# Kernel optimization log

Hardware: AMD Instinct MI355X
Metric: run time of the kernel (lower is better)

The kernel has to match this reference:

```python
import jax, jax.numpy as jnp
import numpy as np
from jax import lax

B, Q, H, W = 2, 2304, 64, 64
ENC_OUT = 64          # encoder out_dim
DIM = 192             # base_dim
HEAD = 8
R = 3
RA = (2 * R + 1) ** 2  # 49 local-window positions
CF = 64                # pe enc_dims // 2 (complex channels)
ENC_DIMS = 2 * CF      # 128
IN_DIM = (DIM + ENC_DIMS) * RA + 2  # 15682
HID = 256


def conv3(x, w, b):
    y = lax.conv_general_dilated(x, w, (1, 1), 'SAME',
                                 dimension_numbers=('NCHW', 'OIHW', 'NCHW'))
    return y + b[None, :, None, None]


def _flat_gather(img, idx):
    # img [B,C,HW], idx [B,...] -> [B,C,...]
    return jax.vmap(lambda f, i: f[:, i])(img, idx)


def gather_nearest(img, c):
    # grid_sample nearest, align_corners=False, zeros padding. c [B,Q,K,2] (y,x)
    Bc, C, Hc, Wc = img.shape
    py = ((c[..., 0] + 1) * Hc - 1) / 2
    px = ((c[..., 1] + 1) * Wc - 1) / 2
    iy = jnp.round(py); ix = jnp.round(px)
    valid = (iy >= 0) & (iy < Hc) & (ix >= 0) & (ix < Wc)
    idx = (jnp.clip(iy, 0, Hc - 1) * Wc + jnp.clip(ix, 0, Wc - 1)).astype(jnp.int32)
    g = _flat_gather(img.reshape(Bc, C, Hc * Wc), idx)  # [B,C,Q,K]
    g = jnp.where(valid[:, None], g, 0.0)
    return g.transpose(0, 2, 3, 1)  # [B,Q,K,C]


def gather_bilinear_zeros(img, c):
    # grid_sample bilinear, align_corners=False, zeros padding. c [B,Q,K,2]
    Bc, C, Hc, Wc = img.shape
    py = ((c[..., 0] + 1) * Hc - 1) / 2
    px = ((c[..., 1] + 1) * Wc - 1) / 2
    y0f = jnp.floor(py); x0f = jnp.floor(px)
    wy = py - y0f; wx = px - x0f
    y0 = y0f.astype(jnp.int32); x0 = x0f.astype(jnp.int32)
    flat = img.reshape(Bc, C, Hc * Wc)
    def corner(yi, xi, w):
        valid = (yi >= 0) & (yi < Hc) & (xi >= 0) & (xi < Wc)
        idx = jnp.clip(yi, 0, Hc - 1) * Wc + jnp.clip(xi, 0, Wc - 1)
        return _flat_gather(flat, idx) * (w * valid)[:, None]
    out = (corner(y0, x0, (1 - wy) * (1 - wx)) + corner(y0, x0 + 1, (1 - wy) * wx)
           + corner(y0 + 1, x0, wy * (1 - wx)) + corner(y0 + 1, x0 + 1, wy * wx))
    return out.transpose(0, 2, 3, 1)


def gather_bilinear_border(img, c):
    # grid_sample bilinear, align_corners=False, border padding. c [B,Q,2]
    Bc, C, Hc, Wc = img.shape
    py = jnp.clip(((c[..., 0] + 1) * Hc - 1) / 2, 0, Hc - 1)
    px = jnp.clip(((c[..., 1] + 1) * Wc - 1) / 2, 0, Wc - 1)
    y0f = jnp.floor(py); x0f = jnp.floor(px)
    wy = py - y0f; wx = px - x0f
    y0 = y0f.astype(jnp.int32); x0 = x0f.astype(jnp.int32)
    y1 = jnp.minimum(y0 + 1, Hc - 1); x1 = jnp.minimum(x0 + 1, Wc - 1)
    flat = img.reshape(Bc, C, Hc * Wc)
    g = lambda yi, xi: _flat_gather(flat, yi * Wc + xi)  # [B,C,Q]
    out = (g(y0, x0) * ((1 - wy) * (1 - wx))[:, None]
           + g(y0, x1) * ((1 - wy) * wx)[:, None]
           + g(y1, x0) * (wy * (1 - wx))[:, None]
           + g(y1, x1) * (wy * wx)[:, None])
    return out.transpose(0, 2, 1)  # [B,Q,C]


def _forward(inp, coord, cell, enc_w, enc_b, qw, qb, kw, kb, vw, vb, fw, fb,
             pbw, pbb, pew, w1, b1, w2, b2):
    feat = conv3(inp, enc_w, enc_b)            # encoder (simplified)
    fq = conv3(feat, qw, qb); fk = conv3(feat, kw, kb)
    fv = conv3(feat, vw, vb); ff = conv3(feat, fw, fb)
    Bq, Qn = coord.shape[:2]
    Hf, Wf = feat.shape[-2:]
    dk = DIM // HEAD
    c = jnp.clip(coord, -1 + 1e-6, 1 - 1e-6)[:, :, None, :]   # [B,Q,1,2]
    # nearest feature-grid pixel-center coordinates (= grid_sample nearest of coord_lr)
    iy = jnp.round(((c[..., 0] + 1) * Hf - 1) / 2)
    ix = jnp.round(((c[..., 1] + 1) * Wf - 1) / 2)
    ck0 = jnp.stack([-1 + (2 * iy + 1) / Hf, -1 + (2 * ix + 1) / Wf], axis=-1)
    dh = jnp.linspace(-R, R, 2 * R + 1) * 2 / Hf
    dw = jnp.linspace(-R, R, 2 * R + 1) * 2 / Wf
    delta = jnp.stack(jnp.meshgrid(dh, dw, indexing='ij'), axis=-1).reshape(1, 1, RA, 2)
    ck = ck0 + delta                                          # [B,Q,49,2]
    q_ = gather_bilinear_zeros(fq, c)[:, :, 0].reshape(Bq, Qn, HEAD, dk)
    k_ = gather_nearest(fk, ck).reshape(Bq, Qn, RA, HEAD, dk)
    v_ = gather_nearest(fv, ck).reshape(Bq, Qn, RA, HEAD, dk)
    fr = gather_nearest(ff, ck)                               # [B,Q,49,CF]
    hw = jnp.array([Hf, Wf], dtype=coord.dtype)
    rel = (coord[:, :, None, :] - ck) * hw                    # [B,Q,49,2]
    rel_cell = cell * hw
    sim = jnp.einsum('bqhd,bqkhd->bqkh', q_, k_) / np.sqrt(dk).astype(np.float32)
    pb = rel @ pbw + pbb                                      # positional bias [B,Q,49,HEAD]
    attn = jax.nn.softmax(sim + pb, axis=2)                   # softmax over the 49 window slots
    attn_map = attn[0, 10, :, 0].reshape(2 * R + 1, 2 * R + 1, 1)
    v_weighted = (v_ * attn[..., None]).reshape(Bq, Qn, RA, DIM)
    frc = jnp.fft.fft2(fr.reshape(Bq, Qn, 2 * R + 1, 2 * R + 1, CF),
                       axes=(2, 3), norm='ortho').reshape(Bq, Qn, RA, CF)
    phase = rel @ pew                                         # Fourier PE: exp(i*phase)
    enc = lax.complex(jnp.cos(phase), jnp.sin(phase)) * frc
    enc = jnp.stack([enc.real, enc.imag], axis=-1).reshape(Bq, Qn, RA, ENC_DIMS)
    out = jnp.concatenate([v_weighted, enc], axis=-1).reshape(Bq, Qn, -1)
    out = jnp.concatenate([out, rel_cell], axis=-1)           # [B,Q,IN_DIM]
    pred = jax.nn.relu(out @ w1 + b1) @ w2 + b2               # imnet MLP
    ret = pred + gather_bilinear_border(inp, coord)           # global residual
    return ret, attn_map


def setup_inputs() -> dict:
    key = jax.random.key(0)
    ks = jax.random.split(key, 20)
    def n(k, shape, s=0.05):
        return jax.random.normal(k, shape, dtype=jnp.float32) * s
    inp = jax.random.normal(ks[0], (B, 3, H, W), dtype=jnp.float32)
    coord = jax.random.uniform(ks[1], (B, Q, 2), minval=-1.0, maxval=1.0, dtype=jnp.float32)
    cell = jnp.full((B, Q, 2), 2.0 / 128, dtype=jnp.float32)
    return {
        'inp': inp, 'coord': coord, 'cell': cell,
        'enc_w': n(ks[2], (ENC_OUT, 3, 3, 3)), 'enc_b': n(ks[3], (ENC_OUT,)),
        'qw': n(ks[4], (DIM, ENC_OUT, 3, 3)), 'qb': n(ks[5], (DIM,)),
        'kw': n(ks[6], (DIM, ENC_OUT, 3, 3)), 'kb': n(ks[7], (DIM,)),
        'vw': n(ks[8], (DIM, ENC_OUT, 3, 3)), 'vb': n(ks[9], (DIM,)),
        'fw': n(ks[10], (CF, ENC_OUT, 3, 3)), 'fb': n(ks[11], (CF,)),
        'pbw': n(ks[12], (2, HEAD), 0.5), 'pbb': n(ks[13], (HEAD,), 0.5),
        'pew': n(ks[14], (2, CF), 0.5),
        'w1': n(ks[15], (IN_DIM, HID), 0.01), 'b1': n(ks[16], (HID,)),
        'w2': n(ks[17], (HID, 3), 0.05), 'b2': n(ks[18], (3,)),
    }


def reference(inp, coord, cell, enc_w, enc_b, qw, qb, kw, kb, vw, vb, fw, fb,
              pbw, pbb, pew, w1, b1, w2, b2):
    return _forward(inp, coord, cell, enc_w, enc_b, qw, qb, kw, kb, vw, vb,
                    fw, fb, pbw, pbb, pew, w1, b1, w2, b2)
```

## Files before the change

### kernel.cpp

```cpp
#include <hip/hip_runtime.h>

typedef unsigned short u16t;
typedef unsigned int   u32t;
typedef __attribute__((ext_vector_type(8))) short short8;
typedef __attribute__((ext_vector_type(4))) float f32x4;

#define B_    2
#define QN    2304
#define NQ    4608
#define HWS   64
#define ENCC  64
#define DIMC  192
#define NHEAD 8
#define DKH   24
#define RAW   49
#define CFC   64
#define FRP   68
#define CMAP  640
#define KCONV 576
#define INDIM 15682
#define KPAD  16128
#define HIDN  256
#define PIX   8192
#define SPLITK 12
#define KSLICE (KPAD/SPLITK)

__device__ __forceinline__ float b2f(u16t u){ u32t v=((u32t)u)<<16; return __builtin_bit_cast(float,v); }
__device__ __forceinline__ u16t f2b(float f){ u32t v=__builtin_bit_cast(u32t,f); return (u16t)((v + 0x7FFFu + ((v>>16)&1u))>>16); }

#define GLOAD16(SRC, DST) __builtin_amdgcn_global_load_lds( \
  (const __attribute__((address_space(1))) unsigned int*)(const void*)(SRC), \
  (__attribute__((address_space(3))) unsigned int*)(void*)(DST), 16, 0, 0)

__global__ __launch_bounds__(256) void k_enc(const float* __restrict__ inp, const float* __restrict__ ew,
                      const float* __restrict__ eb, u16t* __restrict__ feat){
  int i = blockIdx.x*256+threadIdx.x;
  if(i>=B_*HWS*HWS*ENCC) return;
  int oc=i&63, x=(i>>6)&63, y=(i>>12)&63, b=i>>18;
  float acc = eb[oc];
  for(int c=0;c<3;c++)
    for(int dy=0;dy<3;dy++){
      int yy=y+dy-1; if(yy<0||yy>=HWS) continue;
      for(int dx=0;dx<3;dx++){
        int xx=x+dx-1; if(xx<0||xx>=HWS) continue;
        acc += inp[((b*3+c)*HWS+yy)*HWS+xx] * ew[((oc*3+c)*3+dy)*3+dx];
      }
    }
  feat[i]=f2b(acc);
}

__global__ __launch_bounds__(256) void k_w1t(const float* __restrict__ w1, u16t* __restrict__ w1t){
  __shared__ u16t t[64][65];
  int kb = blockIdx.x*64, nb = blockIdx.y*64;
  for(int i=threadIdx.x;i<4096;i+=256){
    int k=i>>6, n=i&63; int gk=kb+k;
    t[k][n] = (gk<INDIM) ? f2b(w1[(size_t)gk*HIDN + nb + n]) : (u16t)0;
  }
  __syncthreads();
  for(int i=threadIdx.x;i<4096;i+=256){
    int n=i>>6, k=i&63;
    w1t[(size_t)(nb+n)*KPAD + kb + k] = t[k][n];
  }
}

__global__ __launch_bounds__(256) void k_wconv(const float* qw,const float* kw,const float* vw,const float* fw,
                        const float* qb,const float* kb_,const float* vb,const float* fb,
                        u16t* __restrict__ wct, float* __restrict__ bias){
  int i = blockIdx.x*256+threadIdx.x;
  if(i < CMAP*KCONV){
    int oc=i/KCONV, kk=i%KCONV;
    int ic=kk&63, tap=kk>>6;
    const float* w; int ol=oc;
    if(oc<192) w=qw;
    else if(oc<384){w=kw; ol=oc-192;}
    else if(oc<576){w=vw; ol=oc-384;}
    else {w=fw; ol=oc-576;}
    wct[(size_t)oc*KCONV + kk] = f2b(w[(ol*64+ic)*9 + tap]);
  }
  if(i<CMAP){
    bias[i] = (i<192)? qb[i] : (i<384? kb_[i-192] : (i<576? vb[i-384] : fb[i-576]));
  }
}

__global__ __launch_bounds__(256) void k_im2col(const u16t* __restrict__ feat, u16t* __restrict__ A){
  int i = blockIdx.x*256+threadIdx.x;
  if(i>=PIX*72) return;
  int k8=i%72, pix=i/72;
  int tap=k8/8, ic8=(k8&7)<<3;
  int x=pix&63, y=(pix>>6)&63, b=pix>>12;
  int yy=y+tap/3-1, xx=x+tap%3-1;
  uint4 v;
  if(yy>=0&&yy<HWS&&xx>=0&&xx<HWS) v = *(const uint4*)&feat[(size_t)(((b*HWS+yy)*HWS+xx)*ENCC)+ic8];
  else v = make_uint4(0u,0u,0u,0u);
  *(uint4*)&A[(size_t)pix*KCONV + tap*64 + ic8] = v;
}

__global__ __launch_bounds__(256) void k_gemm128(const u16t* __restrict__ A, int lda,
    const u16t* __restrict__ BT, int ldb, const float* __restrict__ bias,
    void* __restrict__ Cout, int ldc, int kslice, int mode){
  __shared__ __align__(16) u16t As[128*64];
  __shared__ __align__(16) u16t Bs[128*64];
  int m0 = blockIdx.x*128, n0 = blockIdx.y*128;
  int tid = threadIdx.x;
  int wave = tid>>6, lane = tid&63;
  int wm = wave>>1, wn = wave&1;
  int kg = lane>>4, l16 = lane&15;
  int kbeg = blockIdx.z*kslice, kend = kbeg+kslice;
  f32x4 acc[4][4] = {};
  for(int k0=kbeg;k0<kend;k0+=64){
    __syncthreads();
    #pragma unroll
    for(int j=0;j<4;j++){
      int seg = (wave*4+j)*64 + lane;
      int row = seg>>3, qp = seg&7;
      int q = qp ^ (row&7);
      GLOAD16(&A [(size_t)(m0+row)*lda + k0 + q*8], &As[(wave*4+j)*512]);
      GLOAD16(&BT[(size_t)(n0+row)*ldb + k0 + q*8], &Bs[(wave*4+j)*512]);
    }
    __syncthreads();
    #pragma unroll
    for(int kk=0;kk<2;kk++){
      int ks = kk*4 + kg;
      short8 a[4], b[4];
      #pragma unroll
      for(int mf=0;mf<4;mf++){
        int row = wm*64+mf*16+l16;
        a[mf] = *(const short8*)&As[row*64 + (ks^(row&7))*8];
      }
      #pragma unroll
      for(int nf=0;nf<4;nf++){
        int row = wn*64+nf*16+l16;
        b[nf] = *(const short8*)&Bs[row*64 + (ks^(row&7))*8];
      }
      #pragma unroll
      for(int mf=0;mf<4;mf++)
        #pragma unroll
        for(int nf=0;nf<4;nf++)
          acc[mf][nf] = __builtin_amdgcn_mfma_f32_16x16x32_bf16(a[mf], b[nf], acc[mf][nf], 0,0,0);
    }
  }
  int l4 = lane>>4;
  if(mode==0){
    u16t* C16 = (u16t*)Cout;
    #pragma unroll
    for(int mf=0;mf<4;mf++){
      #pragma unroll
      for(int nf=0;nf<4;nf++){
        #pragma unroll
        for(int r=0;r<4;r++){
          int gm = m0 + wm*64 + mf*16 + l4*4 + r;
          int gn = n0 + wn*64 + nf*16 + l16;
          C16[(size_t)gm*ldc+gn] = f2b(acc[mf][nf][r] + bias[gn]);
        }
      }
    }
  } else {
    u16t* C16 = (u16t*)Cout + (size_t)blockIdx.z * (size_t)(gridDim.x*128) * ldc;
    #pragma unroll
    for(int mf=0;mf<4;mf++){
      #pragma unroll
      for(int nf=0;nf<4;nf++){
        #pragma unroll
        for(int r=0;r<4;r++){
          int gm = m0 + wm*64 + mf*16 + l4*4 + r;
          int gn = n0 + wn*64 + nf*16 + l16;
          C16[(size_t)gm*ldc+gn] = f2b(acc[mf][nf][r]);
        }
      }
    }
  }
}

__global__ __launch_bounds__(256) void k_redout(const u16t* __restrict__ hidp, const float* __restrict__ b1,
                      const float* __restrict__ w2, const float* __restrict__ b2v,
                      const float* __restrict__ inp, const float* __restrict__ coord,
                      float* __restrict__ outp, int M, int q0){
  int i = blockIdx.x*256+threadIdx.x;
  if(i>=M*64) return;
  int q=i>>6, lane=i&63, n4=lane*4;
  f32x4 acc = *(const f32x4*)&b1[n4];
  for(int s=0;s<SPLITK;s++){
    uint2 t = *(const uint2*)&hidp[((size_t)s*M + q)*HIDN + n4];
    acc.x += b2f((u16t)t.x); acc.y += b2f((u16t)(t.x>>16));
    acc.z += b2f((u16t)t.y); acc.w += b2f((u16t)(t.y>>16));
  }
  float h0=fmaxf(acc.x,0.f), h1=fmaxf(acc.y,0.f), h2=fmaxf(acc.z,0.f), h3=fmaxf(acc.w,0.f);
  float p0 = h0*w2[n4*3+0] + h1*w2[(n4+1)*3+0] + h2*w2[(n4+2)*3+0] + h3*w2[(n4+3)*3+0];
  float p1 = h0*w2[n4*3+1] + h1*w2[(n4+1)*3+1] + h2*w2[(n4+2)*3+1] + h3*w2[(n4+3)*3+1];
  float p2 = h0*w2[n4*3+2] + h1*w2[(n4+1)*3+2] + h2*w2[(n4+2)*3+2] + h3*w2[(n4+3)*3+2];
  #pragma unroll
  for(int m=1;m<64;m<<=1){
    p0 += __shfl_xor(p0, m);
    p1 += __shfl_xor(p1, m);
    p2 += __shfl_xor(p2, m);
  }
  if(lane<3){
    int qg = q0 + q;
    int j = lane;
    float accj = (j==0? p0 : (j==1? p1 : p2)) + b2v[j];
    int b=qg/QN;
    float cy=coord[qg*2], cx=coord[qg*2+1];
    float py=fminf(fmaxf(((cy+1.f)*64.f-1.f)*0.5f,0.f),63.f);
    float px=fminf(fmaxf(((cx+1.f)*64.f-1.f)*0.5f,0.f),63.f);
    float y0f=floorf(py), x0f=floorf(px);
    float wy=py-y0f, wx=px-x0f;
    int y0=(int)y0f, x0=(int)x0f;
    int y1=min(y0+1,63), x1=min(x0+1,63);
    const float* ip=&inp[(size_t)(b*3+j)*4096];
    float g00=ip[y0*64+x0], g01=ip[y0*64+x1];
    float g10=ip[y1*64+x0], g11=ip[y1*64+x1];
    float res=g00*(1.f-wy)*(1.f-wx)+g01*(1.f-wy)*wx+g10*wy*(1.f-wx)+g11*wy*wx;
    outp[qg*3+j]=accj+res;
  }
}

__global__ __launch_bounds__(256,8) void k_feat(const float* __restrict__ coord, const float* __restrict__ cell,
                       const u16t* __restrict__ maps, const float* __restrict__ pbw,
                       const float* __restrict__ pbb, const float* __restrict__ pew,
                       u16t* __restrict__ F, float* __restrict__ outAttn, int q0){
  __shared__ float q_lds[DIMC];
  __shared__ float relsy[RAW], relsx[RAW];
  __shared__ int   wbase[RAW];
  __shared__ float sa[RAW][NHEAD];
  __shared__ float fr_lds[RAW*FRP];
  __shared__ float c7[7], s7[7];
  __shared__ float pewf0[CFC], pewf1[CFC];
  __shared__ float pbwf0[NHEAD], pbwf1[NHEAD], pbbf[NHEAD];

  int qg = q0 + blockIdx.x;
  int b  = qg / QN;
  int tid = threadIdx.x;
  float cy = coord[qg*2], cx = coord[qg*2+1];
  const float lo = -1.0f + 1e-6f, hi = 1.0f - 1e-6f;
  float ccy = fminf(fmaxf(cy,lo),hi), ccx = fminf(fmaxf(cx,lo),hi);
  float pyq = ((ccy+1.f)*64.f - 1.f)*0.5f, pxq = ((ccx+1.f)*64.f - 1.f)*0.5f;
  int iy = (int)rintf(pyq), ix = (int)rintf(pxq);

  if(tid < RAW){
    int ki = tid/7, kj = tid%7;
    int yy = iy + ki - 3, xx = ix + kj - 3;
    wbase[tid] = (yy>=0&&yy<64&&xx>=0&&xx<64) ? ((b*64+yy)*64+xx)*CMAP : -1;
    float ck_y = (-1.f + (float)(2*iy+1)*(1.f/64.f)) + (float)(ki-3)*(2.f/64.f);
    float ck_x = (-1.f + (float)(2*ix+1)*(1.f/64.f)) + (float)(kj-3)*(2.f/64.f);
    relsy[tid] = (cy - ck_y)*64.f;
    relsx[tid] = (cx - ck_x)*64.f;
  }
  if(tid<7){ float ang = -6.283185307179586f * (float)tid / 7.f; c7[tid]=cosf(ang); s7[tid]=sinf(ang); }
  if(tid<CFC){ pewf0[tid]=pew[tid]; pewf1[tid]=pew[CFC+tid]; }
  if(tid<NHEAD){ pbwf0[tid]=pbw[tid]; pbwf1[tid]=pbw[NHEAD+tid]; pbbf[tid]=pbb[tid]; }
  __syncthreads();

  if(tid < DIMC){
    float y0f=floorf(pyq), x0f=floorf(pxq);
    float wy=pyq-y0f, wx=pxq-x0f;
    int y0=(int)y0f, x0=(int)x0f;
    float acc=0.f;
    for(int ty=0;ty<2;ty++) for(int tx=0;tx<2;tx++){
      int yy=y0+ty, xx=x0+tx;
      if(yy<0||yy>=64||xx<0||xx>=64) continue;
      float w=(ty? wy:1.f-wy)*(tx? wx:1.f-wx);
      acc += w * b2f(maps[(size_t)((b*64+yy)*64+xx)*CMAP + tid]);
    }
    q_lds[tid]=acc;
  }
  for(int i=tid;i<RAW*8;i+=256){
    int k=i>>3, c8=(i&7)<<3;
    int base=wbase[k];
    f32x4 lo4={0.f,0.f,0.f,0.f}, hi4={0.f,0.f,0.f,0.f};
    if(base>=0){
      uint4 t = *(const uint4*)&maps[(size_t)base + 576 + c8];
      lo4 = f32x4{b2f((u16t)t.x), b2f((u16t)(t.x>>16)), b2f((u16t)t.y), b2f((u16t)(t.y>>16))};
      hi4 = f32x4{b2f((u16t)t.z), b2f((u16t)(t.z>>16)), b2f((u16t)t.w), b2f((u16t)(t.w>>16))};
    }
    *(f32x4*)&fr_lds[k*FRP+c8]   = lo4;
    *(f32x4*)&fr_lds[k*FRP+c8+4] = hi4;
  }
  __syncthreads();

  for(int i=tid;i<RAW*NHEAD;i+=256){
    int k=i>>3, h=i&7;
    int base=wbase[k];
    float dot=0.f;
    if(base>=0){
      const u16t* p = &maps[(size_t)base + DIMC + h*DKH];
      for(int c8=0;c8<3;c8++){
        uint4 t = *(const uint4*)&p[c8*8];
        u32t a4[4]={t.x,t.y,t.z,t.w};
        for(int j=0;j<4;j++){
          dot += q_lds[h*DKH + c8*8 + 2*j]   * b2f((u16t)a4[j]);
          dot += q_lds[h*DKH + c8*8 + 2*j+1] * b2f((u16t)(a4[j]>>16));
        }
      }
    }
    sa[k][h] = dot/sqrtf(24.f) + relsy[k]*pbwf0[h] + relsx[k]*pbwf1[h] + pbbf[h];
  }
  __syncthreads();

  if(tid < 64){
    int h = tid>>3, sub = tid&7;
    float m = -1e30f;
    for(int k=sub;k<RAW;k+=8) m = fmaxf(m, sa[k][h]);
    #pragma unroll
    for(int mm=1;mm<8;mm<<=1) m = fmaxf(m, __shfl_xor(m, mm));
    float s = 0.f;
    for(int k=sub;k<RAW;k+=8){ float e=__expf(sa[k][h]-m); sa[k][h]=e; s+=e; }
    #pragma unroll
    for(int mm=1;mm<8;mm<<=1) s += __shfl_xor(s, mm);
    float inv = 1.f/s;
    for(int k=sub;k<RAW;k+=8) sa[k][h]*=inv;
  }
  __syncthreads();
  if(qg==10 && tid<RAW) outAttn[tid] = sa[tid][0];

  size_t frow = (size_t)(qg-q0)*KPAD;
  for(int i=tid;i<RAW*24;i+=256){
    int k=i/24, c8=(i%24)*8;
    int base=wbase[k];
    u32t o[4]={0,0,0,0};
    if(base>=0){
      uint4 t = *(const uint4*)&maps[(size_t)base + 384 + c8];
      u32t a4[4]={t.x,t.y,t.z,t.w};
      for(int j=0;j<4;j++){
        int c0=c8+2*j;
        u16t r0=f2b(b2f((u16t)a4[j])      * sa[k][ c0   /DKH]);
        u16t r1=f2b(b2f((u16t)(a4[j]>>16))* sa[k][(c0+1)/DKH]);
        o[j] = (u32t)r0 | ((u32t)r1<<16);
      }
    }
    *(uint4*)&F[frow + (size_t)k*320 + c8] = make_uint4(o[0],o[1],o[2],o[3]);
  }
  for(int idx=INDIM-2+tid; idx<KPAD; idx+=256){
    u16t v=0;
    if(idx==15680) v=f2b(cell[qg*2]*64.f);
    else if(idx==15681) v=f2b(cell[qg*2+1]*64.f);
    F[frow+idx]=v;
  }

  #pragma unroll
  for(int pp=0;pp<2;pp++){
    int p = tid + pp*256;
    if(p < 448){
      int v_ = p>>6, c = p&63;
      float Gr[7], Gi[7];
      #pragma unroll
      for(int a_=0;a_<7;a_++){
        float re=0.f, im=0.f;
        #pragma unroll
        for(int bb=0;bb<7;bb++){
          float f=fr_lds[(a_*7+bb)*FRP+c];
          int m=(v_*bb)%7;
          re += f*c7[m]; im += f*s7[m];
        }
        Gr[a_]=re; Gi[a_]=im;
      }
      float pw0=pewf0[c], pw1=pewf1[c];
      #pragma unroll
      for(int u=0;u<7;u++){
        int k = u*7 + v_;
        float tr=0.f, ti=0.f;
        #pragma unroll
        for(int a_=0;a_<7;a_++){
          int m=(u*a_)%7;
          float cc=c7[m], ss=s7[m];
          tr += Gr[a_]*cc - Gi[a_]*ss;
          ti += Gr[a_]*ss + Gi[a_]*cc;
        }
        tr*=(1.f/7.f); ti*=(1.f/7.f);
        float ph = relsy[k]*pw0 + relsx[k]*pw1;
        float sp, cp; __sincosf(ph, &sp, &cp);
        float er = cp*tr - sp*ti, ei = cp*ti + sp*tr;
        u32t pk = (u32t)f2b(er) | ((u32t)f2b(ei)<<16);
        *(u32t*)&F[frow + (size_t)k*320 + 192 + 2*c] = pk;
      }
    }
  }
}

__global__ __launch_bounds__(256) void k_mark(float* __restrict__ outp, int n, float val){
  int i = blockIdx.x*256+threadIdx.x;
  if(i<n) outp[i]=val;
}

extern "C" void kernel_launch(void* const* d_in, const int* in_sizes, int n_in,
                              void* d_out, int out_size, void* d_ws, size_t ws_size,
                              hipStream_t stream){
  int I_inp, I_coord, I_cell, I_encw, I_encb, I_qw, I_qb, I_kw, I_kb, I_vw, I_vb,
      I_fw, I_fb, I_pbw, I_pbb, I_pew, I_w1, I_b1, I_w2, I_b2;
  bool dictOrder = (n_in==20 && in_sizes[0]==24576 && in_sizes[1]==9216 && in_sizes[3]==1728
                    && in_sizes[5]==110592 && in_sizes[16]==4014592 && in_sizes[19]==3);
  bool sortOrder = (n_in==20 && in_sizes[0]==256 && in_sizes[1]==3 && in_sizes[8]==24576
                    && in_sizes[10]==110592 && in_sizes[18]==4014592 && in_sizes[19]==768);
  if(dictOrder){
    I_inp=0; I_coord=1; I_cell=2; I_encw=3; I_encb=4; I_qw=5; I_qb=6; I_kw=7; I_kb=8;
    I_vw=9; I_vb=10; I_fw=11; I_fb=12; I_pbw=13; I_pbb=14; I_pew=15; I_w1=16; I_b1=17; I_w2=18; I_b2=19;
  } else if(sortOrder){
    I_b1=0; I_b2=1; I_cell=2; I_coord=3; I_encb=4; I_encw=5; I_fb=6; I_fw=7; I_inp=8;
    I_kb=9; I_kw=10; I_pbb=11; I_pbw=12; I_pew=13; I_qb=14; I_qw=15; I_vb=16; I_vw=17; I_w1=18; I_w2=19;
  } else {
    float mark = (float)(n_in==20 ? in_sizes[0] : 1000000+n_in);
    k_mark<<<dim3((out_size+255)/256), dim3(256), 0, stream>>>((float*)d_out, out_size, mark);
    return;
  }

  const float* inp  =(const float*)d_in[I_inp];
  const float* coord=(const float*)d_in[I_coord];
  const float* cell =(const float*)d_in[I_cell];
  const float* enc_w=(const float*)d_in[I_encw];
  const float* enc_b=(const float*)d_in[I_encb];
  const float* qw=(const float*)d_in[I_qw];
  const float* qb=(const float*)d_in[I_qb];
  const float* kw=(const float*)d_in[I_kw];
  const float* kbp=(const float*)d_in[I_kb];
  const float* vw=(const float*)d_in[I_vw];
  const float* vb=(const float*)d_in[I_vb];
  const float* fw=(const float*)d_in[I_fw];
  const float* fb=(const float*)d_in[I_fb];
  const float* pbw=(const float*)d_in[I_pbw];
  const float* pbb=(const float*)d_in[I_pbb];
  const float* pew=(const float*)d_in[I_pew];
  const float* w1=(const float*)d_in[I_w1];
  const float* b1=(const float*)d_in[I_b1];
  const float* w2=(const float*)d_in[I_w2];
  const float* b2v=(const float*)d_in[I_b2];
  float* outp=(float*)d_out;

  char* ws=(char*)d_ws;
  size_t off=0;
  auto alloc=[&](size_t bytes){ size_t o=off; off=(off+bytes+255)&~(size_t)255; return o; };
  size_t o_feat = alloc((size_t)PIX*ENCC*2);
  size_t o_imc  = alloc((size_t)PIX*KCONV*2);
  size_t o_wct  = alloc((size_t)CMAP*KCONV*2);
  size_t o_cb   = alloc((size_t)CMAP*4);
  size_t o_maps = alloc((size_t)PIX*CMAP*2);
  size_t o_w1t  = alloc((size_t)HIDN*KPAD*2);
  size_t fixed = off;
  size_t rem = (ws_size>fixed)? ws_size-fixed : 0;
  size_t perQ = (size_t)KPAD*2 + (size_t)SPLITK*HIDN*2;
  long long cq = (long long)(rem/perQ);
  int chunkQ = (int)((cq/128)*128);
  if(chunkQ>NQ) chunkQ=NQ;
  size_t o_F, o_hp;
  if(chunkQ>=128){
    o_F  = alloc((size_t)chunkQ*KPAD*2);
    o_hp = alloc((size_t)SPLITK*chunkQ*HIDN*2);
  } else {
    chunkQ = 128;
    o_F  = o_imc;
    o_hp = (o_imc + (size_t)128*KPAD*2 + 255) & ~(size_t)255;
  }

  u16t*  feat=(u16t*)(ws+o_feat);
  u16t*  imc =(u16t*)(ws+o_imc);
  u16t*  wct =(u16t*)(ws+o_wct);
  float* cbias=(float*)(ws+o_cb);
  u16t*  maps=(u16t*)(ws+o_maps);
  u16t*  w1t =(u16t*)(ws+o_w1t);
  u16t*  Fb  =(u16t*)(ws+o_F);
  u16t*  hidp=(u16t*)(ws+o_hp);

  k_w1t   <<<dim3(KPAD/64, HIDN/64), dim3(256), 0, stream>>>(w1, w1t);
  k_wconv <<<dim3((CMAP*KCONV+255)/256), dim3(256), 0, stream>>>(qw,kw,vw,fw,qb,kbp,vb,fb,wct,cbias);
  k_enc   <<<dim3((PIX*ENCC+255)/256), dim3(256), 0, stream>>>(inp,enc_w,enc_b,feat);
  k_im2col<<<dim3((PIX*72+255)/256), dim3(256), 0, stream>>>(feat,imc);
  k_gemm128<<<dim3(PIX/128, CMAP/128, 1), dim3(256), 0, stream>>>(imc, KCONV, wct, KCONV, cbias,
            (void*)maps, CMAP, KCONV, 0);

  for(int q0=0;q0<NQ;q0+=chunkQ){
    int nq = (NQ-q0 < chunkQ) ? (NQ-q0) : chunkQ;
    k_feat<<<dim3(nq), dim3(256), 0, stream>>>(coord,cell,maps,pbw,pbb,pew,Fb,outp+13824,q0);
    k_gemm128<<<dim3(nq/128, HIDN/128, SPLITK), dim3(256), 0, stream>>>(Fb, KPAD, w1t, KPAD, b1,
            (void*)hidp, HIDN, KSLICE, 2);
    k_redout<<<dim3((nq*64+255)/256), dim3(256), 0, stream>>>(hidp, b1, w2, b2v, inp, coord,
            outp, nq, q0);
  }
}
```

Measured before the change: 184.6 us.

## Add dedicated 64x256 MLP GEMM kernel so each A tile is loaded once

Replaces the generic 128x128 split-K GEMM for the first MLP layer with a specialised kernel. Each block now covers 64 query rows and all 256 hidden outputs, so the large feature matrix A is read once instead of twice across two N tiles. The cost is that the whole 256x64 weight slice is reloaded per block and the grid gets more, smaller M blocks. It also uses a swizzled LDS layout and a per-wave N split.

```diff
diff --git a/kernel.cpp b/kernel.cpp
--- a/kernel.cpp
+++ b/kernel.cpp
@@ -166,6 +166,70 @@
           int gn = n0 + wn*64 + nf*16 + l16;
           C16[(size_t)gm*ldc+gn] = f2b(acc[mf][nf][r]);
         }
+      }
+    }
+  }
+}
+
+__global__ __launch_bounds__(256) void k_gemmMLP(const u16t* __restrict__ A, int lda,
+    const u16t* __restrict__ BT, int ldb, u16t* __restrict__ Cout, int kslice){
+  __shared__ __align__(16) u16t As[64*64];
+  __shared__ __align__(16) u16t Bs[256*64];
+  int m0 = blockIdx.x*64;
+  int tid = threadIdx.x;
+  int wave = tid>>6, lane = tid&63;
+  int kg = lane>>4, l16 = lane&15;
+  int kbeg = blockIdx.z*kslice, kend = kbeg+kslice;
+  f32x4 acc[4][4] = {};
+  for(int k0=kbeg;k0<kend;k0+=64){
+    __syncthreads();
+    #pragma unroll
+    for(int j=0;j<2;j++){
+      int seg = (wave*2+j)*64 + lane;
+      int row = seg>>3, qp = seg&7;
+      int q = qp ^ (row&7);
+      GLOAD16(&A[(size_t)(m0+row)*lda + k0 + q*8], &As[(wave*2+j)*512]);
+    }
+    #pragma unroll
+    for(int j=0;j<8;j++){
+      int seg = (wave*8+j)*64 + lane;
+      int row = seg>>3, qp = seg&7;
+      int q = qp ^ (row&7);
+      GLOAD16(&BT[(size_t)row*ldb + k0 + q*8], &Bs[(wave*8+j)*512]);
+    }
+    __syncthreads();
+    #pragma unroll
+    for(int kk=0;kk<2;kk++){
+      int ks = kk*4 + kg;
+      short8 a[4], b[4];
+      #pragma unroll
+      for(int mf=0;mf<4;mf++){
+        int row = mf*16+l16;
+        a[mf] = *(const short8*)&As[row*64 + (ks^(row&7))*8];
+      }
+      #pragma unroll
+      for(int nf=0;nf<4;nf++){
+        int row = wave*64+nf*16+l16;
+        b[nf] = *(const short8*)&Bs[row*64 + (ks^(row&7))*8];
+      }
+      #pragma unroll
+      for(int mf=0;mf<4;mf++)
+        #pragma unroll
+        for(int nf=0;nf<4;nf++)
+          acc[mf][nf] = __builtin_amdgcn_mfma_f32_16x16x32_bf16(a[mf], b[nf], acc[mf][nf], 0,0,0);
+    }
+  }
+  int l4 = lane>>4;
+  u16t* C16 = Cout + (size_t)blockIdx.z * (size_t)(gridDim.x*64) * HIDN;
+  #pragma unroll
+  for(int mf=0;mf<4;mf++){
+    #pragma unroll
+    for(int nf=0;nf<4;nf++){
+      #pragma unroll
+      for(int r=0;r<4;r++){
+        int gm = m0 + mf*16 + l4*4 + r;
+        int gn = wave*64 + nf*16 + l16;
+        C16[(size_t)gm*HIDN+gn] = f2b(acc[mf][nf][r]);
       }
     }
   }
@@ -468,8 +532,7 @@
   for(int q0=0;q0<NQ;q0+=chunkQ){
     int nq = (NQ-q0 < chunkQ) ? (NQ-q0) : chunkQ;
     k_feat<<<dim3(nq), dim3(256), 0, stream>>>(coord,cell,maps,pbw,pbb,pew,Fb,outp+13824,q0);
-    k_gemm128<<<dim3(nq/128, HIDN/128, SPLITK), dim3(256), 0, stream>>>(Fb, KPAD, w1t, KPAD, b1,
-            (void*)hidp, HIDN, KSLICE, 2);
+    k_gemmMLP<<<dim3(nq/64, 1, SPLITK), dim3(256), 0, stream>>>(Fb, KPAD, w1t, KPAD, hidp, KSLICE);
     k_redout<<<dim3((nq*64+255)/256), dim3(256), 0, stream>>>(hidp, b1, w2, b2v, inp, coord,
             outp, nq, q0);
   }
```

After: 183.3 us. No clear change (-0.7%).
